# Optimization experiments

Measured on AMD Instinct MI355X. Metric: run time of the kernel, lower is better.

## Reference

```python
import jax, jax.numpy as jnp
import numpy as np

A0 = 0.529177249
SIGMA = jnp.array([0.5515909, 1.8886297, 1.3225029, 1.2316629, 2.1884933, 1.7750372, 1.3677907, 1.3820058], dtype=jnp.float32)

N_MOL, N_ATOM, AEV_LEN = 256, 384, 384
DIMS = [160, 128, 96]


def _mlp(x, W1, b1, W2, b2, W3, b3, W4, b4):
    celu = lambda v: jax.nn.celu(v, alpha=0.1)
    h = celu(x @ W1.T + b1)
    h = celu(h @ W2.T + b2)
    h = celu(h @ W3.T + b3)
    return jax.nn.softplus(h @ W4.T + b4)  # (Nn, 1)


def setup_inputs() -> dict:
    key = jax.random.key(0)
    ks = jax.random.split(key, 12)
    species = jax.random.randint(ks[0], (N_MOL, N_ATOM), 0, 8)
    # pad the tail of each molecule (species == -1)
    species = species.at[:, N_ATOM - 64:].set(-1)
    coordinates = jax.random.normal(ks[1], (N_MOL, N_ATOM, 3), dtype=jnp.float32) * 3.0
    net_charge = jax.random.normal(ks[2], (N_MOL,), dtype=jnp.float32)
    aev = jax.random.normal(ks[3], (N_MOL, N_ATOM, AEV_LEN), dtype=jnp.float32)
    in_dim = AEV_LEN + 2
    d1, d2, d3 = DIMS
    s = 0.05
    W1 = jax.random.normal(ks[4], (d1, in_dim), dtype=jnp.float32) * s
    b1 = jnp.zeros((d1,), dtype=jnp.float32)
    W2 = jax.random.normal(ks[5], (d2, d1), dtype=jnp.float32) * s
    b2 = jnp.zeros((d2,), dtype=jnp.float32)
    W3 = jax.random.normal(ks[6], (d3, d2), dtype=jnp.float32) * s
    b3 = jnp.zeros((d3,), dtype=jnp.float32)
    W4 = jax.random.normal(ks[7], (1, d3), dtype=jnp.float32) * s
    b4 = jnp.zeros((1,), dtype=jnp.float32)
    return {"species": species, "coordinates": coordinates, "net_charge": net_charge,
            "aev": aev, "W1": W1, "b1": b1, "W2": W2, "b2": b2,
            "W3": W3, "b3": b3, "W4": W4, "b4": b4}


def reference(species, coordinates, net_charge, aev, W1, b1, W2, b2, W3, b3, W4, b4):
    N, n = species.shape
    # pairwise distances in atomic units (eps avoids div-by-zero on diagonal)
    diff = coordinates[:, None, :, :] - coordinates[:, :, None, :]  # (N,n,n,3)
    distances = jnp.sqrt(jnp.sum(diff * diff, axis=-1) + 1e-16) / A0  # (N,n,n)

    padding_mask = (species != -1).astype(coordinates.dtype)  # (N,n)
    pair_mask = padding_mask[:, :, None] * padding_mask[:, None, :]  # (N,n,n)
    num_atoms = padding_mask.sum(axis=1)  # (N,)

    # ESP kernel j_ij (constant across iterations)
    sig = SIGMA[species]  # negative padding index wraps to last sigma, as in torch
    sig_sqsum = jnp.maximum(sig[:, None, :] ** 2 + sig[:, :, None] ** 2, 1e-8)
    j_ij = jax.lax.erf(distances / jnp.sqrt(2.0 * sig_sqsum)) / distances  # (N,n,n)
    diag_mask = 1.0 - jnp.eye(n, dtype=coordinates.dtype)
    j_masked = j_ij * pair_mask * diag_mask[None]  # fuse masks once

    mask_flat = species.reshape(-1) != -1  # (N*n,)
    aev_flat = aev.reshape(N * n, -1)
    pred_charges = jnp.zeros((N * n,), dtype=coordinates.dtype)
    esp = jnp.zeros((N * n,), dtype=coordinates.dtype)

    for _ in range(4):
        feats = jnp.concatenate(
            [aev_flat, pred_charges[:, None], esp[:, None]], axis=1)  # (Nn, aev+2)
        chi_all = _mlp(feats, W1, b1, W2, b2, W3, b3, W4, b4)[:, 0]
        chi = jnp.where(mask_flat, chi_all, 0.0)  # padded atoms keep 0 (masked_scatter)
        chi_copy = chi.reshape(N, n)
        chi_sum = chi_copy.sum(axis=-1)  # (N,)
        k_net = 1.0 + jnp.abs(net_charge) / chi_sum
        chi_mean = chi_sum / num_atoms
        k_p = jnp.where(net_charge > 0, k_net, 1.0)
        k_n = jnp.where(net_charge < 0, k_net, 1.0)
        iter_charges = (-k_n[:, None] * chi_copy + (k_p * chi_mean)[:, None]) * padding_mask
        # esp_j = sum_i q_i * j_ij[i, j] (masked)
        esp2d = jnp.sum(iter_charges[:, :, None] * j_masked, axis=1)  # (N,n)
        pred_charges = iter_charges.reshape(-1)
        esp = esp2d.reshape(-1)

    return species, pred_charges.reshape(N, n)
```

## Files before the change

### kernel.cpp

```cpp
#include <hip/hip_runtime.h>
#include <math.h>

#define NMOL 256
#define NATOM 384
#define NN (NMOL*NATOM)
#define A0C  0.529177249f
#define A0_INV (1.0f/0.529177249f)

typedef short bf16x8 __attribute__((ext_vector_type(8)));
typedef float f32x4  __attribute__((ext_vector_type(4)));

__constant__ float c_sigma[8] = {0.5515909f, 1.8886297f, 1.3225029f, 1.2316629f,
                                 2.1884933f, 1.7750372f, 1.3677907f, 1.3820058f};

__device__ __forceinline__ short f2b(float f) {
    unsigned u = __float_as_uint(f);
    u = (u + 0x7fffu + ((u >> 16) & 1u)) >> 16;
    return (short)u;
}
__device__ __forceinline__ float b2f(short s) {
    return __uint_as_float(((unsigned)(unsigned short)s) << 16);
}
__device__ __forceinline__ float celu01(float v) {
    float e = __builtin_amdgcn_exp2f(v * 14.426950408889634f);
    return v > 0.f ? v : fmaf(0.1f, e, -0.1f);
}
__device__ __forceinline__ bf16x8 cvt8(f32x4 a, f32x4 b) {
    bf16x8 r;
    r[0] = f2b(a.x); r[1] = f2b(a.y); r[2] = f2b(a.z); r[3] = f2b(a.w);
    r[4] = f2b(b.x); r[5] = f2b(b.y); r[6] = f2b(b.z); r[7] = f2b(b.w);
    return r;
}

__device__ __forceinline__ float erf_fast(float x) {
    float t = __builtin_amdgcn_rcpf(fmaf(0.3275911f, x, 1.0f));
    float p = fmaf(t, 1.061405429f, -1.453152027f);
    p = fmaf(t, p, 1.421413741f);
    p = fmaf(t, p, -0.284496736f);
    p = fmaf(t, p, 0.254829592f);
    p = p * t;
    float e = __builtin_amdgcn_exp2f(-x * x * 1.4426950408889634f);
    return fmaf(-p, e, 1.0f);
}

template<int N, int K>
__global__ __launch_bounds__(256, 4)
void gemm0_k(const float* __restrict__ A, const short* __restrict__ Bw,
             const float* __restrict__ bias, short* __restrict__ Cout)
{
    constexpr int NK = K / 32;
    constexpr int NF = N / 32;
    constexpr int N2 = N / 2;
    constexpr int AROW = 40, BROW = 40;
    constexpr int ASZ = 64 * AROW;
    constexpr int BSZ = N * BROW;
    constexpr int AB  = 2 * ASZ + 2 * BSZ;
    constexpr int CSZ = 64 * N;
    constexpr int SM  = AB > CSZ ? AB : CSZ;
    constexpr int NB  = (N * 4 + 255) / 256;

    __shared__ short smem[SM];
    short* As0 = smem;
    short* As1 = smem + ASZ;
    short* Bs0 = smem + 2 * ASZ;
    short* Bs1 = smem + 2 * ASZ + BSZ;
    short* Cs  = smem;

    const int t    = threadIdx.x;
    const int lane = t & 63;
    const int wave = t >> 6;
    const int wm   = wave >> 1, wn = wave & 1;
    const int l15  = lane & 15, l4 = lane >> 4;
    const int m0   = blockIdx.x * 64;
    const int arow = t >> 2, aseg = t & 3;
    const float* a_f32 = A + ((size_t)m0 + arow) * K + aseg * 8;

    f32x4 af0, af1;
    bf16x8 br[NB];

    auto loadA = [&](int k0) {
        af0 = *(const f32x4*)(a_f32 + k0);
        af1 = *(const f32x4*)(a_f32 + k0 + 4);
    };
    auto loadB = [&](int k0) {
        #pragma unroll
        for (int ci = 0; ci < NB; ++ci) {
            int c = ci * 256 + t;
            if ((N * 4) % 256 == 0 || c < N * 4) {
                int row = c >> 2, half = c & 3;
                br[ci] = *(const bf16x8*)(Bw + (size_t)row * K + k0 + half * 8);
            }
        }
    };
    auto writeA = [&](short* dst) {
        *(bf16x8*)&dst[arow * AROW + aseg * 8] = cvt8(af0, af1);
    };
    auto writeB = [&](short* dst) {
        #pragma unroll
        for (int ci = 0; ci < NB; ++ci) {
            int c = ci * 256 + t;
            if ((N * 4) % 256 == 0 || c < N * 4) {
                int row = c >> 2, half = c & 3;
                *(bf16x8*)&dst[row * BROW + half * 8] = br[ci];
            }
        }
    };

    f32x4 acc[2][NF] = {};

    loadA(0); loadB(0);
    writeA(As0); writeB(Bs0);
    __syncthreads();

    int cur = 0;
    for (int ks = 0; ks < NK; ++ks) {
        if (ks + 1 < NK) { loadA((ks + 1) * 32); loadB((ks + 1) * 32); }
        short* Ac = cur ? As1 : As0;
        short* Bc = cur ? Bs1 : Bs0;
        bf16x8 a[2];
        #pragma unroll
        for (int mf = 0; mf < 2; ++mf)
            a[mf] = *(const bf16x8*)&Ac[(wm * 32 + mf * 16 + l15) * AROW + l4 * 8];
        #pragma unroll
        for (int nf = 0; nf < NF; ++nf) {
            bf16x8 b = *(const bf16x8*)&Bc[(wn * N2 + nf * 16 + l15) * BROW + l4 * 8];
            #pragma unroll
            for (int mf = 0; mf < 2; ++mf)
                acc[mf][nf] = __builtin_amdgcn_mfma_f32_16x16x32_bf16(a[mf], b, acc[mf][nf], 0, 0, 0);
        }
        if (ks + 1 < NK) {
            writeA(cur ? As0 : As1);
            writeB(cur ? Bs0 : Bs1);
            __syncthreads();
            cur ^= 1;
        }
    }
    __syncthreads();

    #pragma unroll
    for (int nf = 0; nf < NF; ++nf) {
        int col = wn * N2 + nf * 16 + l15;
        float bc = bias[col];
        #pragma unroll
        for (int mf = 0; mf < 2; ++mf)
            #pragma unroll
            for (int r = 0; r < 4; ++r)
                Cs[(wm * 32 + mf * 16 + l4 * 4 + r) * N + col] = f2b(acc[mf][nf][r] + bc);
    }
    __syncthreads();
    #pragma unroll
    for (int i = 0; i < NF; ++i) {
        int c = i * 256 + t;
        *(bf16x8*)(Cout + (size_t)m0 * N + c * 8) = *(const bf16x8*)&Cs[c * 8];
    }
}

__global__ __launch_bounds__(256, 4)
void mlp23_kernel(const short* __restrict__ h1p, const short* __restrict__ W2b,
                  const float* __restrict__ b2, const short* __restrict__ W3b,
                  const float* __restrict__ b3, const float* __restrict__ W4,
                  const float* __restrict__ b4,
                  const float* __restrict__ qv, const float* __restrict__ espv,
                  const float* __restrict__ w1qp, const float* __restrict__ w1ep,
                  const int* __restrict__ species, float* __restrict__ chi)
{
    constexpr int K1 = 160, K2 = 128, N3 = 96;
    constexpr int H2ROW = 140;

    __shared__ short H2[64 * H2ROW];
    __shared__ float wq_s[K1], we_s[K1], w4_s[N3], b3_s[N3];
    __shared__ float chp[2][64];

    const int t    = threadIdx.x;
    const int lane = t & 63;
    const int wave = t >> 6;
    const int wm   = wave >> 1, wn = wave & 1;
    const int l15  = lane & 15, l4 = lane >> 4;
    const int m0   = blockIdx.x * 64;

    if (t < K1) { wq_s[t] = w1qp[t]; we_s[t] = w1ep[t]; }
    if (t < N3) { w4_s[t] = W4[t]; b3_s[t] = b3[t]; }

    int rowg[2];
    float qrow[2], erow[2];
    #pragma unroll
    for (int mf = 0; mf < 2; ++mf) {
        rowg[mf] = m0 + wm * 32 + mf * 16 + l15;
        qrow[mf] = qv[rowg[mf]];
        erow[mf] = espv[rowg[mf]];
    }
    __syncthreads();

    f32x4 acc[2][4] = {};
    #pragma unroll
    for (int ks = 0; ks < 5; ++ks) {
        const int k0 = ks * 32 + l4 * 8;
        f32x4 wq0 = *(const f32x4*)&wq_s[k0];
        f32x4 wq1 = *(const f32x4*)&wq_s[k0 + 4];
        f32x4 we0 = *(const f32x4*)&we_s[k0];
        f32x4 we1 = *(const f32x4*)&we_s[k0 + 4];
        bf16x8 a[2];
        #pragma unroll
        for (int mf = 0; mf < 2; ++mf) {
            bf16x8 h = *(const bf16x8*)(h1p + (size_t)rowg[mf] * K1 + k0);
            #pragma unroll
            for (int j = 0; j < 4; ++j) {
                float v  = b2f(h[j])     + qrow[mf] * wq0[j] + erow[mf] * we0[j];
                float v2 = b2f(h[j + 4]) + qrow[mf] * wq1[j] + erow[mf] * we1[j];
                a[mf][j]     = f2b(celu01(v));
                a[mf][j + 4] = f2b(celu01(v2));
            }
        }
        #pragma unroll
        for (int nf = 0; nf < 4; ++nf) {
            bf16x8 b = *(const bf16x8*)(W2b + (size_t)(wn * 64 + nf * 16 + l15) * K1 + k0);
            #pragma unroll
            for (int mf = 0; mf < 2; ++mf)
                acc[mf][nf] = __builtin_amdgcn_mfma_f32_16x16x32_bf16(a[mf], b, acc[mf][nf], 0, 0, 0);
        }
    }

    #pragma unroll
    for (int nf = 0; nf < 4; ++nf) {
        int col = wn * 64 + nf * 16 + l15;
        float bc = b2[col];
        #pragma unroll
        for (int mf = 0; mf < 2; ++mf)
            #pragma unroll
            for (int r = 0; r < 4; ++r)
                H2[(wm * 32 + mf * 16 + l4 * 4 + r) * H2ROW + col] =
                    f2b(celu01(acc[mf][nf][r] + bc));
    }
    __syncthreads();

    f32x4 acc2[2][3] = {};
    #pragma unroll
    for (int ks = 0; ks < 4; ++ks) {
        bf16x8 a[2];
        #pragma unroll
        for (int mf = 0; mf < 2; ++mf)
            a[mf] = *(const bf16x8*)&H2[(wm * 32 + mf * 16 + l15) * H2ROW + ks * 32 + l4 * 8];
        #pragma unroll
        for (int nf = 0; nf < 3; ++nf) {
            bf16x8 b = *(const bf16x8*)(W3b + (size_t)(wn * 48 + nf * 16 + l15) * K2 + ks * 32 + l4 * 8);
            #pragma unroll
            for (int mf = 0; mf < 2; ++mf)
                acc2[mf][nf] = __builtin_amdgcn_mfma_f32_16x16x32_bf16(a[mf], b, acc2[mf][nf], 0, 0, 0);
        }
    }

    float val[2][4];
    #pragma unroll
    for (int mf = 0; mf < 2; ++mf)
        #pragma unroll
        for (int r = 0; r < 4; ++r) val[mf][r] = 0.f;
    #pragma unroll
    for (int nf = 0; nf < 3; ++nf) {
        int col = wn * 48 + nf * 16 + l15;
        float bc = b3_s[col];
        float wc = w4_s[col];
        #pragma unroll
        for (int mf = 0; mf < 2; ++mf)
            #pragma unroll
            for (int r = 0; r < 4; ++r)
                val[mf][r] += celu01(acc2[mf][nf][r] + bc) * wc;
    }
    #pragma unroll
    for (int off = 1; off < 16; off <<= 1)
        #pragma unroll
        for (int mf = 0; mf < 2; ++mf)
            #pragma unroll
            for (int r = 0; r < 4; ++r)
                val[mf][r] += __shfl_xor(val[mf][r], off, 64);
    if (l15 == 0) {
        #pragma unroll
        for (int mf = 0; mf < 2; ++mf)
            #pragma unroll
            for (int r = 0; r < 4; ++r)
                chp[wn][wm * 32 + mf * 16 + l4 * 4 + r] = val[mf][r];
    }
    __syncthreads();
    if (t < 64) {
        float s = chp[0][t] + chp[1][t] + b4[0];
        s = fmaxf(s, 0.f) + log1pf(expf(-fabsf(s)));
        chi[m0 + t] = (species[m0 + t] != -1) ? s : 0.f;
    }
}

template<bool DO_ESP>
__global__ __launch_bounds__(384, 6)
void espd_kernel(const float* __restrict__ chi, const int* __restrict__ species,
                 const float* __restrict__ netq, const float* __restrict__ coords,
                 float* __restrict__ q, float* __restrict__ esp,
                 float* __restrict__ out)
{
    __shared__ float q_s[NATOM], msk_s[NATOM];
    __shared__ float cxs[NATOM], cys[NATOM], czs[NATOM], s2s[NATOM];
    __shared__ float part[NATOM];
    __shared__ float red_s[6], redc_s[6];

    const int m  = blockIdx.x, jt = blockIdx.y;
    const int t  = threadIdx.x;
    const int lane = t & 63, wv = t >> 6;
    const int idx = m * NATOM + t;

    float c = chi[idx];
    int sp = species[idx];
    float mk = (sp != -1) ? 1.f : 0.f;
    msk_s[t] = mk;
    if (DO_ESP) {
        cxs[t] = coords[(size_t)idx * 3 + 0];
        cys[t] = coords[(size_t)idx * 3 + 1];
        czs[t] = coords[(size_t)idx * 3 + 2];
        float sig = c_sigma[sp < 0 ? 7 : sp];
        s2s[t] = sig * sig;
    }
    float sc = c, sm = mk;
    #pragma unroll
    for (int off = 1; off < 64; off <<= 1) {
        sc += __shfl_xor(sc, off, 64);
        sm += __shfl_xor(sm, off, 64);
    }
    if (lane == 0) { red_s[wv] = sc; redc_s[wv] = sm; }
    __syncthreads();
    float chi_sum = red_s[0] + red_s[1] + red_s[2] + red_s[3] + red_s[4] + red_s[5];
    float na      = redc_s[0] + redc_s[1] + redc_s[2] + redc_s[3] + redc_s[4] + redc_s[5];
    float Q = netq[m];
    float k_net = 1.f + fabsf(Q) / chi_sum;
    float chi_mean = chi_sum / na;
    float k_p = (Q > 0.f) ? k_net : 1.f;
    float k_n = (Q < 0.f) ? k_net : 1.f;
    float qj = (-k_n * c + k_p * chi_mean) * mk;

    if (!DO_ESP) {
        out[idx]      = (float)sp;
        out[NN + idx] = qj;
        return;
    }

    q_s[t] = qj;
    if (jt == 0) q[idx] = qj;
    __syncthreads();

    const int joff = t % 96;
    const int iq   = t / 96;
    const int jj   = jt * 96 + joff;
    const float rx = cxs[jj], ry = cys[jj], rz = czs[jj], s2j = s2s[jj];
    float acc = 0.f;
    const int i0 = iq * 96;
    #pragma unroll 4
    for (int i = i0; i < i0 + 96; ++i) {
        float dx = cxs[i] - rx, dy = cys[i] - ry, dz = czs[i] - rz;
        float d2 = fmaf(dx, dx, fmaf(dy, dy, dz * dz)) + 1e-16f;
        float rs = __builtin_amdgcn_rsqf(d2);
        float d  = d2 * rs * A0_INV;
        float ss = fmaxf(s2s[i] + s2j, 1e-8f);
        float x  = d * __builtin_amdgcn_rsqf(2.f * ss);
        float v  = erf_fast(x) * rs * A0C;
        acc += (i == jj) ? 0.f : q_s[i] * v;
    }
    part[t] = acc;
    __syncthreads();
    if (t < 96) {
        float s = part[t] + part[t + 96] + part[t + 192] + part[t + 288];
        esp[m * NATOM + jt * 96 + t] = (msk_s[jt * 96 + t] != 0.f) ? s : 0.f;
    }
}

__global__ __launch_bounds__(256)
void wcvt_kernel(const float* __restrict__ W1, const float* __restrict__ W2,
                 const float* __restrict__ W3,
                 short* __restrict__ W1b, short* __restrict__ W2b,
                 short* __restrict__ W3b, float* __restrict__ w1q,
                 float* __restrict__ w1e)
{
    int i = blockIdx.x * 256 + threadIdx.x;
    if (i < 160 * 384) {
        int r = i / 384, cc = i % 384;
        W1b[i] = f2b(W1[(size_t)r * 386 + cc]);
    }
    int j = i - 160 * 384;
    if (j >= 0 && j < 128 * 160) W2b[j] = f2b(W2[j]);
    int k2 = j - 128 * 160;
    if (k2 >= 0 && k2 < 96 * 128) W3b[k2] = f2b(W3[k2]);
    if (i < 160) {
        w1q[i] = W1[(size_t)i * 386 + 384];
        w1e[i] = W1[(size_t)i * 386 + 385];
    }
}

extern "C" void kernel_launch(void* const* d_in, const int* in_sizes, int n_in,
                              void* d_out, int out_size, void* d_ws, size_t ws_size,
                              hipStream_t stream)
{
    const int*   species = (const int*)  d_in[0];
    const float* coords  = (const float*)d_in[1];
    const float* netq    = (const float*)d_in[2];
    const float* aev     = (const float*)d_in[3];
    const float* W1 = (const float*)d_in[4];
    const float* b1 = (const float*)d_in[5];
    const float* W2 = (const float*)d_in[6];
    const float* b2 = (const float*)d_in[7];
    const float* W3 = (const float*)d_in[8];
    const float* b3 = (const float*)d_in[9];
    const float* W4 = (const float*)d_in[10];
    const float* b4 = (const float*)d_in[11];

    float* q    = (float*)d_ws;
    float* esp  = q + NN;
    float* chi  = esp + NN;
    float* w1q  = chi + NN;
    float* w1e  = w1q + 160;
    short* W1b  = (short*)(w1e + 160);
    short* W2b  = W1b + 160 * 384;
    short* W3b  = W2b + 128 * 160;
    short* h1p  = W3b + 96 * 128;

    hipMemsetAsync(q, 0, 2 * (size_t)NN * sizeof(float), stream);
    wcvt_kernel<<<(160 * 384 + 128 * 160 + 96 * 128 + 255) / 256, 256, 0, stream>>>(
        W1, W2, W3, W1b, W2b, W3b, w1q, w1e);

    gemm0_k<160, 384><<<NN / 64, 256, 0, stream>>>(aev, W1b, b1, h1p);

    for (int it = 0; it < 4; ++it) {
        mlp23_kernel<<<NN / 64, 256, 0, stream>>>(
            h1p, W2b, b2, W3b, b3, W4, b4, q, esp, w1q, w1e, species, chi);
        if (it < 3)
            espd_kernel<true><<<dim3(NMOL, 4), 384, 0, stream>>>(
                chi, species, netq, coords, q, esp, nullptr);
        else
            espd_kernel<false><<<dim3(NMOL, 1), 384, 0, stream>>>(
                chi, species, netq, coords, q, esp, (float*)d_out);
    }
}
```

Measured before the change: 286.6 us.

## Precompute fp16 ESP kernel matrix once and reuse it as a matvec each iteration

A new kernel builds the masked pairwise ESP interaction matrix J in fp16 once per call. Each charge-equilibration iteration then runs a matrix-vector product over J instead of recomputing distances and erf. The ESP partial sums go into four slices that the MLP kernel adds together, and mlp23 is reorganised so each wave owns 16 rows across all output columns. This trades repeated transcendental work for a large workspace buffer and its memory traffic, with fp16 rounding of J, and falls back to the old path when the workspace is too small.

Result: slower. 302.9 us (+5.7%).

```diff
diff --git a/kernel.cpp b/kernel.cpp
--- a/kernel.cpp
+++ b/kernel.cpp
@@ -9,6 +9,7 @@
 
 typedef short bf16x8 __attribute__((ext_vector_type(8)));
 typedef float f32x4  __attribute__((ext_vector_type(4)));
+typedef _Float16 h16x8 __attribute__((ext_vector_type(8)));
 
 __constant__ float c_sigma[8] = {0.5515909f, 1.8886297f, 1.3225029f, 1.2316629f,
                                  2.1884933f, 1.7750372f, 1.3677907f, 1.3820058f};
@@ -164,127 +165,189 @@
                   const float* __restrict__ w1qp, const float* __restrict__ w1ep,
                   const int* __restrict__ species, float* __restrict__ chi)
 {
-    constexpr int K1 = 160, K2 = 128, N3 = 96;
-    constexpr int H2ROW = 140;
+    constexpr int K1 = 160, K2 = 128;
+    constexpr int H2ROW = 144;
 
     __shared__ short H2[64 * H2ROW];
-    __shared__ float wq_s[K1], we_s[K1], w4_s[N3], b3_s[N3];
-    __shared__ float chp[2][64];
+    __shared__ float wq_s[K1], we_s[K1];
 
     const int t    = threadIdx.x;
     const int lane = t & 63;
-    const int wave = t >> 6;
-    const int wm   = wave >> 1, wn = wave & 1;
+    const int wv   = t >> 6;
     const int l15  = lane & 15, l4 = lane >> 4;
     const int m0   = blockIdx.x * 64;
+    const int row  = m0 + wv * 16 + l15;
 
     if (t < K1) { wq_s[t] = w1qp[t]; we_s[t] = w1ep[t]; }
-    if (t < N3) { w4_s[t] = W4[t]; b3_s[t] = b3[t]; }
-
-    int rowg[2];
-    float qrow[2], erow[2];
-    #pragma unroll
-    for (int mf = 0; mf < 2; ++mf) {
-        rowg[mf] = m0 + wm * 32 + mf * 16 + l15;
-        qrow[mf] = qv[rowg[mf]];
-        erow[mf] = espv[rowg[mf]];
-    }
-    __syncthreads();
-
-    f32x4 acc[2][4] = {};
+
+    const float qr = qv[row];
+    const float er = espv[row] + espv[NN + row]
+                   + espv[2 * (size_t)NN + row] + espv[3 * (size_t)NN + row];
+    __syncthreads();
+
+    f32x4 acc[8] = {};
     #pragma unroll
     for (int ks = 0; ks < 5; ++ks) {
         const int k0 = ks * 32 + l4 * 8;
-        f32x4 wq0 = *(const f32x4*)&wq_s[k0];
-        f32x4 wq1 = *(const f32x4*)&wq_s[k0 + 4];
-        f32x4 we0 = *(const f32x4*)&we_s[k0];
-        f32x4 we1 = *(const f32x4*)&we_s[k0 + 4];
-        bf16x8 a[2];
-        #pragma unroll
-        for (int mf = 0; mf < 2; ++mf) {
-            bf16x8 h = *(const bf16x8*)(h1p + (size_t)rowg[mf] * K1 + k0);
-            #pragma unroll
-            for (int j = 0; j < 4; ++j) {
-                float v  = b2f(h[j])     + qrow[mf] * wq0[j] + erow[mf] * we0[j];
-                float v2 = b2f(h[j + 4]) + qrow[mf] * wq1[j] + erow[mf] * we1[j];
-                a[mf][j]     = f2b(celu01(v));
-                a[mf][j + 4] = f2b(celu01(v2));
-            }
-        }
-        #pragma unroll
-        for (int nf = 0; nf < 4; ++nf) {
-            bf16x8 b = *(const bf16x8*)(W2b + (size_t)(wn * 64 + nf * 16 + l15) * K1 + k0);
-            #pragma unroll
-            for (int mf = 0; mf < 2; ++mf)
-                acc[mf][nf] = __builtin_amdgcn_mfma_f32_16x16x32_bf16(a[mf], b, acc[mf][nf], 0, 0, 0);
-        }
-    }
-
-    #pragma unroll
-    for (int nf = 0; nf < 4; ++nf) {
-        int col = wn * 64 + nf * 16 + l15;
+        bf16x8 h = *(const bf16x8*)(h1p + (size_t)row * K1 + k0);
+        bf16x8 a;
+        #pragma unroll
+        for (int j = 0; j < 8; ++j) {
+            float v = b2f(h[j]) + qr * wq_s[k0 + j] + er * we_s[k0 + j];
+            a[j] = f2b(celu01(v));
+        }
+        #pragma unroll
+        for (int nf = 0; nf < 8; ++nf) {
+            bf16x8 b = *(const bf16x8*)(W2b + (size_t)(nf * 16 + l15) * K1 + k0);
+            acc[nf] = __builtin_amdgcn_mfma_f32_16x16x32_bf16(a, b, acc[nf], 0, 0, 0);
+        }
+    }
+
+    #pragma unroll
+    for (int nf = 0; nf < 8; ++nf) {
+        int col = nf * 16 + l15;
         float bc = b2[col];
         #pragma unroll
-        for (int mf = 0; mf < 2; ++mf)
-            #pragma unroll
-            for (int r = 0; r < 4; ++r)
-                H2[(wm * 32 + mf * 16 + l4 * 4 + r) * H2ROW + col] =
-                    f2b(celu01(acc[mf][nf][r] + bc));
-    }
-    __syncthreads();
-
-    f32x4 acc2[2][3] = {};
+        for (int r = 0; r < 4; ++r)
+            H2[(wv * 16 + l4 * 4 + r) * H2ROW + col] = f2b(celu01(acc[nf][r] + bc));
+    }
+    __syncthreads();
+
+    f32x4 acc2[6] = {};
     #pragma unroll
     for (int ks = 0; ks < 4; ++ks) {
-        bf16x8 a[2];
-        #pragma unroll
-        for (int mf = 0; mf < 2; ++mf)
-            a[mf] = *(const bf16x8*)&H2[(wm * 32 + mf * 16 + l15) * H2ROW + ks * 32 + l4 * 8];
-        #pragma unroll
-        for (int nf = 0; nf < 3; ++nf) {
-            bf16x8 b = *(const bf16x8*)(W3b + (size_t)(wn * 48 + nf * 16 + l15) * K2 + ks * 32 + l4 * 8);
-            #pragma unroll
-            for (int mf = 0; mf < 2; ++mf)
-                acc2[mf][nf] = __builtin_amdgcn_mfma_f32_16x16x32_bf16(a[mf], b, acc2[mf][nf], 0, 0, 0);
-        }
-    }
-
-    float val[2][4];
-    #pragma unroll
-    for (int mf = 0; mf < 2; ++mf)
-        #pragma unroll
-        for (int r = 0; r < 4; ++r) val[mf][r] = 0.f;
-    #pragma unroll
-    for (int nf = 0; nf < 3; ++nf) {
-        int col = wn * 48 + nf * 16 + l15;
-        float bc = b3_s[col];
-        float wc = w4_s[col];
-        #pragma unroll
-        for (int mf = 0; mf < 2; ++mf)
-            #pragma unroll
-            for (int r = 0; r < 4; ++r)
-                val[mf][r] += celu01(acc2[mf][nf][r] + bc) * wc;
+        bf16x8 a2 = *(const bf16x8*)&H2[(wv * 16 + l15) * H2ROW + ks * 32 + l4 * 8];
+        #pragma unroll
+        for (int nf = 0; nf < 6; ++nf) {
+            bf16x8 b = *(const bf16x8*)(W3b + (size_t)(nf * 16 + l15) * K2 + ks * 32 + l4 * 8);
+            acc2[nf] = __builtin_amdgcn_mfma_f32_16x16x32_bf16(a2, b, acc2[nf], 0, 0, 0);
+        }
+    }
+
+    float val[4] = {};
+    #pragma unroll
+    for (int nf = 0; nf < 6; ++nf) {
+        int col = nf * 16 + l15;
+        float bc = b3[col], wc = W4[col];
+        #pragma unroll
+        for (int r = 0; r < 4; ++r)
+            val[r] += celu01(acc2[nf][r] + bc) * wc;
     }
     #pragma unroll
     for (int off = 1; off < 16; off <<= 1)
         #pragma unroll
-        for (int mf = 0; mf < 2; ++mf)
-            #pragma unroll
-            for (int r = 0; r < 4; ++r)
-                val[mf][r] += __shfl_xor(val[mf][r], off, 64);
+        for (int r = 0; r < 4; ++r)
+            val[r] += __shfl_xor(val[r], off, 64);
     if (l15 == 0) {
-        #pragma unroll
-        for (int mf = 0; mf < 2; ++mf)
-            #pragma unroll
-            for (int r = 0; r < 4; ++r)
-                chp[wn][wm * 32 + mf * 16 + l4 * 4 + r] = val[mf][r];
-    }
-    __syncthreads();
-    if (t < 64) {
-        float s = chp[0][t] + chp[1][t] + b4[0];
-        s = fmaxf(s, 0.f) + log1pf(expf(-fabsf(s)));
-        chi[m0 + t] = (species[m0 + t] != -1) ? s : 0.f;
-    }
+        float bb = b4[0];
+        #pragma unroll
+        for (int r = 0; r < 4; ++r) {
+            int rr = m0 + wv * 16 + l4 * 4 + r;
+            float s = val[r] + bb;
+            s = fmaxf(s, 0.f) + log1pf(expf(-fabsf(s)));
+            chi[rr] = (species[rr] != -1) ? s : 0.f;
+        }
+    }
+}
+
+__global__ __launch_bounds__(384)
+void jbuild_kernel(const float* __restrict__ coords, const int* __restrict__ species,
+                   _Float16* __restrict__ J)
+{
+    __shared__ float cx[NATOM], cy[NATOM], cz[NATOM], s2[NATOM], mk[NATOM];
+    int m = blockIdx.x, it0 = blockIdx.y * 48;
+    int j = threadIdx.x;
+    int idx = m * NATOM + j;
+    float rx = coords[(size_t)idx * 3 + 0];
+    float ry = coords[(size_t)idx * 3 + 1];
+    float rz = coords[(size_t)idx * 3 + 2];
+    int sp = species[idx];
+    float sig = c_sigma[sp < 0 ? 7 : sp];
+    cx[j] = rx; cy[j] = ry; cz[j] = rz;
+    s2[j] = sig * sig;
+    float maskj = (sp != -1) ? 1.f : 0.f;
+    mk[j] = maskj;
+    __syncthreads();
+    float s2j = s2[j];
+    #pragma unroll 4
+    for (int ii = 0; ii < 48; ++ii) {
+        int i = it0 + ii;
+        float dx = cx[i] - rx, dy = cy[i] - ry, dz = cz[i] - rz;
+        float d2 = fmaf(dx, dx, fmaf(dy, dy, dz * dz)) + 1e-16f;
+        float rs = __builtin_amdgcn_rsqf(d2);
+        float d  = d2 * rs * A0_INV;
+        float ss = fmaxf(s2[i] + s2j, 1e-8f);
+        float x  = d * __builtin_amdgcn_rsqf(2.f * ss);
+        float val = erf_fast(x) * rs * A0C;
+        val *= maskj * mk[i];
+        val = (i == j) ? 0.f : val;
+        J[((size_t)m * NATOM + i) * NATOM + j] = (_Float16)val;
+    }
+}
+
+template<bool DO_MV>
+__global__ __launch_bounds__(384)
+void espmv_kernel(const float* __restrict__ chi, const int* __restrict__ species,
+                  const float* __restrict__ netq, const _Float16* __restrict__ J,
+                  float* __restrict__ q, float* __restrict__ esp_part,
+                  float* __restrict__ out)
+{
+    __shared__ float pw[6], pwc[6];
+    __shared__ float qs[DO_MV ? 96 : 1];
+    __shared__ float part[DO_MV ? 8 : 1][DO_MV ? 384 : 1];
+    int m = blockIdx.x, ic = blockIdx.y;
+    int t = threadIdx.x;
+    int lane = t & 63, wv = t >> 6;
+    int idx = m * NATOM + t;
+    float c = chi[idx];
+    int sp = species[idx];
+    float mask = (sp != -1) ? 1.f : 0.f;
+    float sc = c, sm = mask;
+    #pragma unroll
+    for (int off = 1; off < 64; off <<= 1) {
+        sc += __shfl_xor(sc, off, 64);
+        sm += __shfl_xor(sm, off, 64);
+    }
+    if (lane == 0) { pw[wv] = sc; pwc[wv] = sm; }
+    __syncthreads();
+    float chi_sum = pw[0] + pw[1] + pw[2] + pw[3] + pw[4] + pw[5];
+    float na      = pwc[0] + pwc[1] + pwc[2] + pwc[3] + pwc[4] + pwc[5];
+    float Q = netq[m];
+    float k_net = 1.f + fabsf(Q) / chi_sum;
+    float chi_mean = chi_sum / na;
+    float k_p = (Q > 0.f) ? k_net : 1.f;
+    float k_n = (Q < 0.f) ? k_net : 1.f;
+    float qj = (-k_n * c + k_p * chi_mean) * mask;
+
+    if (!DO_MV) {
+        out[idx]      = (float)sp;
+        out[NN + idx] = qj;
+        return;
+    }
+
+    if (ic == 0) q[idx] = qj;
+    if (t >= ic * 96 && t < ic * 96 + 96) qs[t - ic * 96] = qj;
+    __syncthreads();
+
+    int jv = t % 48, isub = t / 48;
+    int j0 = jv * 8;
+    float acc[8] = {};
+    #pragma unroll 4
+    for (int k = 0; k < 12; ++k) {
+        int il = isub * 12 + k;
+        int i = ic * 96 + il;
+        h16x8 h = *(const h16x8*)&J[((size_t)m * NATOM + i) * NATOM + j0];
+        float qi = qs[il];
+        #pragma unroll
+        for (int r = 0; r < 8; ++r) acc[r] = fmaf(qi, (float)h[r], acc[r]);
+    }
+    #pragma unroll
+    for (int r = 0; r < 8; ++r) part[isub][j0 + r] = acc[r];
+    __syncthreads();
+    float s = 0.f;
+    #pragma unroll
+    for (int g = 0; g < 8; ++g) s += part[g][t];
+    esp_part[(size_t)ic * NN + idx] = s;
 }
 
 template<bool DO_ESP>
@@ -407,29 +470,45 @@
     const float* b4 = (const float*)d_in[11];
 
     float* q    = (float*)d_ws;
-    float* esp  = q + NN;
-    float* chi  = esp + NN;
+    float* espp = q + NN;
+    float* chi  = espp + 4 * (size_t)NN;
     float* w1q  = chi + NN;
     float* w1e  = w1q + 160;
     short* W1b  = (short*)(w1e + 160);
     short* W2b  = W1b + 160 * 384;
     short* W3b  = W2b + 128 * 160;
     short* h1p  = W3b + 96 * 128;
-
-    hipMemsetAsync(q, 0, 2 * (size_t)NN * sizeof(float), stream);
+    _Float16* J = (_Float16*)(h1p + (size_t)NN * 160);
+
+    const size_t NEED = (size_t)((char*)(J + (size_t)NN * 384) - (char*)d_ws);
+    const bool use_J = (ws_size >= NEED);
+
+    hipMemsetAsync(d_ws, 0, 5 * (size_t)NN * sizeof(float), stream);
     wcvt_kernel<<<(160 * 384 + 128 * 160 + 96 * 128 + 255) / 256, 256, 0, stream>>>(
         W1, W2, W3, W1b, W2b, W3b, w1q, w1e);
 
+    if (use_J)
+        jbuild_kernel<<<dim3(NMOL, 8), 384, 0, stream>>>(coords, species, J);
+
     gemm0_k<160, 384><<<NN / 64, 256, 0, stream>>>(aev, W1b, b1, h1p);
 
     for (int it = 0; it < 4; ++it) {
         mlp23_kernel<<<NN / 64, 256, 0, stream>>>(
-            h1p, W2b, b2, W3b, b3, W4, b4, q, esp, w1q, w1e, species, chi);
-        if (it < 3)
-            espd_kernel<true><<<dim3(NMOL, 4), 384, 0, stream>>>(
-                chi, species, netq, coords, q, esp, nullptr);
-        else
-            espd_kernel<false><<<dim3(NMOL, 1), 384, 0, stream>>>(
-                chi, species, netq, coords, q, esp, (float*)d_out);
-    }
-}
+            h1p, W2b, b2, W3b, b3, W4, b4, q, espp, w1q, w1e, species, chi);
+        if (use_J) {
+            if (it < 3)
+                espmv_kernel<true><<<dim3(NMOL, 4), 384, 0, stream>>>(
+                    chi, species, netq, J, q, espp, nullptr);
+            else
+                espmv_kernel<false><<<dim3(NMOL, 1), 384, 0, stream>>>(
+                    chi, species, netq, J, q, espp, (float*)d_out);
+        } else {
+            if (it < 3)
+                espd_kernel<true><<<dim3(NMOL, 4), 384, 0, stream>>>(
+                    chi, species, netq, coords, q, espp, nullptr);
+            else
+                espd_kernel<false><<<dim3(NMOL, 1), 384, 0, stream>>>(
+                    chi, species, netq, coords, q, espp, (float*)d_out);
+        }
+    }
+}
```
